# Kernel tuning notes

Measured on AMD Instinct MI355X. Metric: run time of the kernel, lower is better.

## Reference

```python
import jax, jax.numpy as jnp
import numpy as np

EPS = 1e-5


def _conv(x, w, pad, groups=1):
    return jax.lax.conv_general_dilated(
        x, w, (1, 1), [(pad, pad), (pad, pad)],
        dimension_numbers=('NCHW', 'OIHW', 'NCHW'),
        feature_group_count=groups)


def _bn(x, p):
    # p: [4, C] = (gamma, beta, running_mean, running_var); eval-mode BatchNorm2d
    g, b, m, v = p
    scale = g / jnp.sqrt(v + EPS)
    return x * scale[None, :, None, None] + (b - m * scale)[None, :, None, None]


def _deform_sample(ir, offset, mask):
    # ir: [B,C,H,W]; offset: [B,18,H,W] interleaved (dy,dx) per 3x3 tap; mask: [B,9,H,W]
    B, C, H, W = ir.shape
    K = 9
    off = offset.reshape(B, K, 2, H, W)
    ky, kx = jnp.meshgrid(jnp.arange(3) - 1, jnp.arange(3) - 1, indexing='ij')
    ys = off[:, :, 0] + ky.reshape(K).astype(ir.dtype)[None, :, None, None] \
         + jnp.arange(H, dtype=ir.dtype)[None, None, :, None]
    xs = off[:, :, 1] + kx.reshape(K).astype(ir.dtype)[None, :, None, None] \
         + jnp.arange(W, dtype=ir.dtype)[None, None, None, :]

    def sample_one(img, ys_b, xs_b):
        # img [C,H,W]; ys_b/xs_b [K,H,W] -> [C,K,H,W]
        y0 = jnp.floor(ys_b); x0 = jnp.floor(xs_b)
        wy = ys_b - y0; wx = xs_b - x0
        y0i = y0.astype(jnp.int32); x0i = x0.astype(jnp.int32)

        def gather(yi, xi):
            valid = (yi >= 0) & (yi < H) & (xi >= 0) & (xi < W)
            v = img[:, jnp.clip(yi, 0, H - 1), jnp.clip(xi, 0, W - 1)]
            return v * valid[None].astype(img.dtype)

        return (gather(y0i, x0i) * ((1 - wy) * (1 - wx))[None]
                + gather(y0i, x0i + 1) * ((1 - wy) * wx)[None]
                + gather(y0i + 1, x0i) * (wy * (1 - wx))[None]
                + gather(y0i + 1, x0i + 1) * (wy * wx)[None])

    vals = jax.vmap(sample_one)(ir, ys, xs)  # [B,C,K,H,W]
    return vals * mask[:, None]  # modulated (DCNv2) sampling


def reference(rgb, ir, w_off1, b_off1, w_off2, b_off2, w_dcn, b_dcn,
              w_g1, bn_g1, w_g2, bn_g2, w_g3, b_g3, w_f, bn_f, res_scale):
    silu = jax.nn.silu
    cat = jnp.concatenate([rgb, ir], axis=1)
    h = silu(_conv(cat, w_off1, 1) + b_off1[None, :, None, None])
    out = _conv(h, w_off2, 1) + b_off2[None, :, None, None]  # [B,27,H,W]
    o1, o2, m = jnp.split(out, 3, axis=1)
    offset = jnp.concatenate([o1, o2], axis=1)  # [B,18,H,W]
    mask = jax.nn.sigmoid(m)                    # [B,9,H,W]

    vals = _deform_sample(ir, offset, mask)     # [B,C,9,H,W]
    Co = w_dcn.shape[0]
    ir_aligned = jnp.einsum('bckhw,ock->bohw', vals, w_dcn.reshape(Co, -1, 9)) \
                 + b_dcn[None, :, None, None]

    mid = w_g2.shape[0]
    g = silu(_bn(_conv(jnp.concatenate([rgb, ir_aligned], axis=1), w_g1, 0), bn_g1))
    g = silu(_bn(_conv(g, w_g2, 1, groups=mid), bn_g2))
    g = jax.nn.sigmoid(_conv(g, w_g3, 0) + b_g3[None, :, None, None])  # [B,1,H,W]

    fused_in = jnp.concatenate([g * ir_aligned, (1.0 - g) * rgb], axis=1)
    fused = silu(_bn(_conv(fused_in, w_f, 1), bn_f))
    return fused + res_scale * ir_aligned


def setup_inputs() -> dict:
    B, CH, H, W = 8, 128, 80, 80
    MID = max(CH // 8, 16)
    key = jax.random.key(0)
    ks = jax.random.split(key, 20)

    def bn_params(k, c):
        k1, k2, k3, k4 = jax.random.split(k, 4)
        gamma = 1.0 + 0.1 * jax.random.normal(k1, (c,), jnp.float32)
        beta = 0.1 * jax.random.normal(k2, (c,), jnp.float32)
        mean = 0.1 * jax.random.normal(k3, (c,), jnp.float32)
        var = jax.random.uniform(k4, (c,), jnp.float32, 0.5, 1.5)
        return jnp.stack([gamma, beta, mean, var])

    return {
        'rgb': jax.random.normal(ks[0], (B, CH, H, W), jnp.float32),
        'ir': jax.random.normal(ks[1], (B, CH, H, W), jnp.float32),
        'w_off1': 0.02 * jax.random.normal(ks[2], (CH, 2 * CH, 3, 3), jnp.float32),
        'b_off1': 0.02 * jax.random.normal(ks[3], (CH,), jnp.float32),
        'w_off2': 0.01 * jax.random.normal(ks[4], (27, CH, 3, 3), jnp.float32),
        'b_off2': 0.01 * jax.random.normal(ks[5], (27,), jnp.float32),
        'w_dcn': 0.03 * jax.random.normal(ks[6], (CH, CH, 3, 3), jnp.float32),
        'b_dcn': 0.03 * jax.random.normal(ks[7], (CH,), jnp.float32),
        'w_g1': 0.05 * jax.random.normal(ks[8], (MID, 2 * CH, 1, 1), jnp.float32),
        'bn_g1': bn_params(ks[9], MID),
        'w_g2': 0.1 * jax.random.normal(ks[10], (MID, 1, 3, 3), jnp.float32),
        'bn_g2': bn_params(ks[11], MID),
        'w_g3': 0.1 * jax.random.normal(ks[12], (1, MID, 1, 1), jnp.float32),
        'b_g3': jnp.ones((1,), jnp.float32),
        'w_f': 0.03 * jax.random.normal(ks[13], (CH, 2 * CH, 3, 3), jnp.float32),
        'bn_f': bn_params(ks[14], CH),
        'res_scale': jnp.array(0.2, jnp.float32),
    }
```

## Files before the change

kernel.cpp:

```cpp
#include <hip/hip_runtime.h>
#include <math.h>

#define HWs 6400

typedef __attribute__((ext_vector_type(8))) short s8v;
typedef __attribute__((ext_vector_type(4))) float f4v;
typedef unsigned short ushortT;
typedef unsigned int uintT;

__device__ __forceinline__ float sigm_(float x){ return 1.0f/(1.0f+__expf(-x)); }
__device__ __forceinline__ float silu_(float x){ return x/(1.0f+__expf(-x)); }
__device__ __forceinline__ ushortT f2bf(float f){
  uintT u = __float_as_uint(f);
  u = (u + 0x7fffu + ((u>>16)&1u)) >> 16;
  return (ushortT)u;
}

__global__ void wtb_kernel(const float* __restrict__ w, ushortT* __restrict__ Bt,
                           int lcin, int OC, int Npad, int K){
  int idx = blockIdx.x*256 + threadIdx.x;
  if (idx >= Npad*K) return;
  int n = idx / K, k = idx - n*K;
  int r = k >> lcin, c = k & ((1<<lcin)-1);
  float v = (n < OC) ? w[(((size_t)n << lcin) + c)*9 + r] : 0.0f;
  Bt[idx] = f2bf(v);
}

__global__ void bnprep_kernel(const float* __restrict__ bn1, const float* __restrict__ bn2,
                              const float* __restrict__ bnf, float* __restrict__ o){
  int t = threadIdx.x;
  if (t < 16){
    float s = bn1[t] / sqrtf(bn1[48+t] + 1e-5f);
    o[t] = s; o[16+t] = bn1[16+t] - bn1[32+t]*s;
  } else if (t < 32){
    int i = t-16;
    float s = bn2[i] / sqrtf(bn2[48+i] + 1e-5f);
    o[32+i] = s; o[48+i] = bn2[16+i] - bn2[32+i]*s;
  } else if (t < 160){
    int i = t-32;
    float s = bnf[i] / sqrtf(bnf[384+i] + 1e-5f);
    o[64+i] = s; o[192+i] = bnf[128+i] - bnf[256+i]*s;
  }
}

template<int MODE, int BN, int EPI, int LCIN>
__global__ __launch_bounds__(256,4)
void mconv(const float* __restrict__ A0, const float* __restrict__ A1,
           int Cin0,
           const float* __restrict__ offp,
           const ushortT* __restrict__ Bt, int K,
           float* __restrict__ Out, int Nout,
           const float* __restrict__ e0, const float* __restrict__ e1,
           const float* __restrict__ res, const float* __restrict__ rsp)
{
  constexpr int CINM = (1<<LCIN) - 1;
  constexpr int MF = (BN==128)? 2 : 1;
  constexpr int NF = (BN==128)? 4 : 2;
  constexpr int BCH = (BN==128)? 2 : 1;
  __shared__ ushortT As[64*40];
  __shared__ ushortT Bs[BN*40];

  const int tid = threadIdx.x;
  const int mb  = blockIdx.x * 64;
  const int b   = mb / HWs;
  const int sm  = tid & 63;
  const int kg  = tid >> 6;
  const int p   = mb - b*HWs + sm;
  const int y   = p / 80;
  const int x   = p - y*80;

  const float* a0p = A0 + (size_t)b*Cin0*HWs + p;
  const float* a1p = (MODE!=1)? (A1 + ((size_t)b*((1<<LCIN)-Cin0) - (size_t)Cin0)*HWs + p) : A0;
  const float* gp  = (MODE==2)? (offp + (size_t)b*HWs + p) : A0;
  const float* ofb = (MODE==1)? (offp + (size_t)b*27*HWs + p) : A0;
  const float* irb = A0 + (size_t)b*128*HWs;

  const int ln  = tid & 63;
  const int l15 = ln & 15, lg = ln >> 4;
  const int wv  = tid >> 6;
  const int wmb = (BN==128)? ((wv>>1)*32) : (wv*16);
  const int wnb = (BN==128)? ((wv&1)*64) : 0;

  f4v acc[MF][NF];
  #pragma unroll
  for (int i=0;i<MF;i++)
    #pragma unroll
    for (int j=0;j<NF;j++)
      #pragma unroll
      for (int q=0;q<4;q++) acc[i][j][q] = 0.0f;

  float w00=0.f,w01=0.f,w10=0.f,w11=0.f;
  int o00=0,o01=0,o10=0,o11=0;
  float gvr = 0.f;

  for (int k0 = 0; k0 < K; k0 += 32){
    const int kb = k0 + kg*8;
    const int r  = kb >> LCIN;
    const int c0 = kb & CINM;
    s8v h;

    if (MODE != 1){
      const int r3 = r/3;
      const int dy = r3 - 1, dx = r - r3*3 - 1;
      const int yy = y + dy, xx = x + dx;
      const bool v = ((unsigned)yy < 80u) & ((unsigned)xx < 80u);
      const float* bp = (c0 < Cin0)? a0p : a1p;
      const float* q = bp + (size_t)c0*HWs + (dy*80 + dx);
      float scl = 1.0f;
      if (MODE == 2){
        if ((k0 & CINM) == 0){
          gvr = v ? gp[dy*80 + dx] : 0.0f;
        }
        scl = (c0 < Cin0)? gvr : (1.0f - gvr);
      }
      if (v){
        #pragma unroll
        for (int kk=0;kk<8;kk++){
          float val = q[(size_t)kk*HWs];
          if (MODE == 2) val *= scl;
          h[kk] = (short)f2bf(val);
        }
      } else {
        #pragma unroll
        for (int kk=0;kk<8;kk++) h[kk] = 0;
      }
    } else {
      if ((k0 & 127) == 0){
        float oy = ofb[(size_t)(2*r)*HWs];
        float ox = ofb[(size_t)(2*r+1)*HWs];
        float mk = sigm_(ofb[(size_t)(18+r)*HWs]);
        int r3 = r/3;
        int dy = r3, dx = r - r3*3;
        float ys = oy + (float)(y + dy - 1);
        float xs = ox + (float)(x + dx - 1);
        float yf = floorf(ys), xf = floorf(xs);
        float wy = ys - yf, wx = xs - xf;
        int y0 = (int)yf, x0 = (int)xf;
        float vy0 = ((unsigned)y0     < 80u)? 1.f : 0.f;
        float vy1 = ((unsigned)(y0+1) < 80u)? 1.f : 0.f;
        float vx0 = ((unsigned)x0     < 80u)? 1.f : 0.f;
        float vx1 = ((unsigned)(x0+1) < 80u)? 1.f : 0.f;
        w00 = (1.f-wy)*(1.f-wx)*mk*vy0*vx0;
        w01 = (1.f-wy)*wx      *mk*vy0*vx1;
        w10 = wy      *(1.f-wx)*mk*vy1*vx0;
        w11 = wy      *wx      *mk*vy1*vx1;
        int cy0 = min(max(y0  ,0),79), cy1 = min(max(y0+1,0),79);
        int cx0 = min(max(x0  ,0),79), cx1 = min(max(x0+1,0),79);
        o00 = cy0*80+cx0; o01 = cy0*80+cx1; o10 = cy1*80+cx0; o11 = cy1*80+cx1;
      }
      const float* q00 = irb + (size_t)c0*HWs + o00;
      const float* q01 = irb + (size_t)c0*HWs + o01;
      const float* q10 = irb + (size_t)c0*HWs + o10;
      const float* q11 = irb + (size_t)c0*HWs + o11;
      #pragma unroll
      for (int kk=0;kk<8;kk++){
        float val = w00*q00[(size_t)kk*HWs] + w01*q01[(size_t)kk*HWs]
                  + w10*q10[(size_t)kk*HWs] + w11*q11[(size_t)kk*HWs];
        h[kk] = (short)f2bf(val);
      }
    }

    uint4 bchunk[BCH];
    #pragma unroll
    for (int i=0;i<BCH;i++){
      int ch = tid + i*256;
      if (BN==128 || tid < 128){
        int n = ch >> 2, kc = (ch & 3) << 3;
        bchunk[i] = *(const uint4*)(Bt + (size_t)n*K + k0 + kc);
      }
    }

    __syncthreads();
    *(s8v*)&As[sm*40 + kg*8] = h;
    #pragma unroll
    for (int i=0;i<BCH;i++){
      int ch = tid + i*256;
      if (BN==128 || tid < 128){
        int n = ch >> 2, kc = (ch & 3) << 3;
        *(uint4*)&Bs[n*40 + kc] = bchunk[i];
      }
    }
    __syncthreads();

    s8v af[MF], bfr[NF];
    #pragma unroll
    for (int i=0;i<MF;i++) af[i]  = *(const s8v*)&As[(wmb + i*16 + l15)*40 + lg*8];
    #pragma unroll
    for (int j=0;j<NF;j++) bfr[j] = *(const s8v*)&Bs[(wnb + j*16 + l15)*40 + lg*8];
    #pragma unroll
    for (int i=0;i<MF;i++)
      #pragma unroll
      for (int j=0;j<NF;j++)
        acc[i][j] = __builtin_amdgcn_mfma_f32_16x16x32_bf16(af[i], bfr[j], acc[i][j], 0, 0, 0);
    __syncthreads();
  }

  float rsv = (EPI==3)? rsp[0] : 0.0f;
  #pragma unroll
  for (int i=0;i<MF;i++){
    int p0 = (mb - b*HWs) + wmb + i*16 + 4*lg;
    #pragma unroll
    for (int j=0;j<NF;j++){
      int n = wnb + j*16 + l15;
      if (BN==32 && n >= Nout) continue;
      size_t ob = ((size_t)b*Nout + n)*HWs + p0;
      float vv[4];
      #pragma unroll
      for (int q=0;q<4;q++) vv[q] = acc[i][j][q];
      if (EPI == 0){
        float bb = e0[n];
        #pragma unroll
        for (int q=0;q<4;q++) vv[q] += bb;
      } else if (EPI == 1){
        float bb = e0[n];
        #pragma unroll
        for (int q=0;q<4;q++) vv[q] = silu_(vv[q] + bb);
      } else if (EPI == 2){
        float s = e0[n], sh = e1[n];
        #pragma unroll
        for (int q=0;q<4;q++) vv[q] = silu_(fmaf(vv[q], s, sh));
      } else {
        float s = e0[n], sh = e1[n];
        float4 r4 = *(const float4*)(res + ob);
        float rr[4] = {r4.x, r4.y, r4.z, r4.w};
        #pragma unroll
        for (int q=0;q<4;q++) vv[q] = silu_(fmaf(vv[q], s, sh)) + rsv*rr[q];
      }
      float4 o4; o4.x=vv[0]; o4.y=vv[1]; o4.z=vv[2]; o4.w=vv[3];
      *(float4*)(Out + ob) = o4;
    }
  }
}

__global__ __launch_bounds__(256) void gate1_kernel(
  const float* __restrict__ rgb, const float* __restrict__ iral,
  const float* __restrict__ wg1, const float* __restrict__ bns,
  float* __restrict__ out)
{
  __shared__ float Ws[4096];
  int tid = threadIdx.x;
  for (int i = tid; i < 4096; i += 256){
    int mc = i >> 8, c = i & 255;
    Ws[c*16 + mc] = wg1[i];
  }
  __syncthreads();
  int idx = blockIdx.x*256 + tid;
  int b = idx / HWs, p = idx - b*HWs;
  const float* r0 = rgb  + (size_t)b*128*HWs + p;
  const float* i0 = iral + ((size_t)b*128 - 128)*HWs + p;
  float acc[16];
  #pragma unroll
  for (int mc=0;mc<16;mc++) acc[mc]=0.f;
  #pragma unroll 4
  for (int c=0;c<256;c++){
    float v = (c<128) ? r0[(size_t)c*HWs] : i0[(size_t)c*HWs];
    const float4* w4 = (const float4*)&Ws[c*16];
    #pragma unroll
    for (int q=0;q<4;q++){
      float4 w = w4[q];
      acc[q*4+0] = fmaf(v, w.x, acc[q*4+0]);
      acc[q*4+1] = fmaf(v, w.y, acc[q*4+1]);
      acc[q*4+2] = fmaf(v, w.z, acc[q*4+2]);
      acc[q*4+3] = fmaf(v, w.w, acc[q*4+3]);
    }
  }
  #pragma unroll
  for (int mc=0;mc<16;mc++){
    float t = fmaf(acc[mc], bns[mc], bns[16+mc]);
    out[((size_t)b*16+mc)*HWs + p] = silu_(t);
  }
}

__global__ __launch_bounds__(256) void gate23_kernel(
  const float* __restrict__ g1b, const float* __restrict__ wg2,
  const float* __restrict__ wg3, const float* __restrict__ bg3,
  const float* __restrict__ bns, float* __restrict__ g)
{
  __shared__ float w2s[144], w3s[16], sc2[16], sh2[16];
  __shared__ float b3s;
  int tid = threadIdx.x;
  if (tid < 144) w2s[tid] = wg2[tid];
  if (tid < 16){ w3s[tid] = wg3[tid]; sc2[tid] = bns[32+tid]; sh2[tid] = bns[48+tid]; }
  if (tid == 0) b3s = bg3[0];
  __syncthreads();
  int idx = blockIdx.x*256 + tid;
  int b = idx / HWs, p = idx - b*HWs;
  int y = p/80, x = p - y*80;
  float acc = b3s;
  #pragma unroll
  for (int mc=0;mc<16;mc++){
    const float* base = g1b + ((size_t)b*16+mc)*HWs;
    float s = 0.f;
    #pragma unroll
    for (int r=0;r<9;r++){
      int dy = r/3, dx = r - (r/3)*3;
      int yy = y + dy - 1, xx = x + dx - 1;
      if (((unsigned)yy < 80u) & ((unsigned)xx < 80u))
        s = fmaf(base[yy*80+xx], w2s[mc*9+r], s);
    }
    float t = fmaf(s, sc2[mc], sh2[mc]);
    acc = fmaf(silu_(t), w3s[mc], acc);
  }
  g[idx] = sigm_(acc);
}

extern "C" void kernel_launch(void* const* d_in, const int* in_sizes, int n_in,
                              void* d_out, int out_size, void* d_ws, size_t ws_size,
                              hipStream_t stream)
{
  const float* rgb  = (const float*)d_in[0];
  const float* ir   = (const float*)d_in[1];
  const float* w1   = (const float*)d_in[2];
  const float* b1   = (const float*)d_in[3];
  const float* w2   = (const float*)d_in[4];
  const float* b2   = (const float*)d_in[5];
  const float* wd   = (const float*)d_in[6];
  const float* bd   = (const float*)d_in[7];
  const float* wg1  = (const float*)d_in[8];
  const float* bng1 = (const float*)d_in[9];
  const float* wg2  = (const float*)d_in[10];
  const float* bng2 = (const float*)d_in[11];
  const float* wg3  = (const float*)d_in[12];
  const float* bg3  = (const float*)d_in[13];
  const float* wf   = (const float*)d_in[14];
  const float* bnf  = (const float*)d_in[15];
  const float* rs   = (const float*)d_in[16];
  float* out = (float*)d_out;

  float* ws   = (float*)d_ws;
  float* hbuf = ws;
  float* offb = hbuf + 6553600;
  float* iral = offb + 1382400;
  float* g1b  = iral + 6553600;
  float* gbuf = g1b  + 819200;
  float* bns  = gbuf + 51200;
  ushortT* Bt1 = (ushortT*)(bns + 320);
  ushortT* Bt2 = Bt1 + 294912;
  ushortT* Bt3 = Bt2 + 36864;
  ushortT* Bt4 = Bt3 + 147456;

  bnprep_kernel<<<1, 256, 0, stream>>>(bng1, bng2, bnf, bns);
  wtb_kernel<<<(294912+255)/256, 256, 0, stream>>>(w1, Bt1, 8, 128, 128, 2304);
  wtb_kernel<<<( 36864+255)/256, 256, 0, stream>>>(w2, Bt2, 7,  27,  32, 1152);
  wtb_kernel<<<(147456+255)/256, 256, 0, stream>>>(wd, Bt3, 7, 128, 128, 1152);
  wtb_kernel<<<(294912+255)/256, 256, 0, stream>>>(wf, Bt4, 8, 128, 128, 2304);

  mconv<0,128,1,8><<<800, 256, 0, stream>>>(rgb, ir, 128, nullptr,
      Bt1, 2304, hbuf, 128, b1, nullptr, nullptr, nullptr);
  mconv<0,32,0,7><<<800, 256, 0, stream>>>(hbuf, hbuf, 128, nullptr,
      Bt2, 1152, offb, 27, b2, nullptr, nullptr, nullptr);
  mconv<1,128,0,7><<<800, 256, 0, stream>>>(ir, ir, 128, offb,
      Bt3, 1152, iral, 128, bd, nullptr, nullptr, nullptr);
  gate1_kernel<<<200, 256, 0, stream>>>(rgb, iral, wg1, bns, g1b);
  gate23_kernel<<<200, 256, 0, stream>>>(g1b, wg2, wg3, bg3, bns, gbuf);
  mconv<2,128,3,8><<<800, 256, 0, stream>>>(iral, rgb, 128, gbuf,
      Bt4, 2304, out, 128, bns+64, bns+192, iral, rs);
}
```

Measured before the change: 928.9 us.

## Reorder im2col K as channel-major with taps padded to sixteen

Changes the GEMM K ordering for the regular 3x3 convolutions so that each channel's 9 taps sit in a 16-wide slot. Each thread loads 8 taps from one channel plane instead of 8 channels at one tap, which gives spatially local loads and per-tap bounds checks. The price is K growing from 2304 to 4096 (and 1152 to 2048), so roughly 78% more MFMA work is spent on zero padding. Blocks are also reindexed so that adjacent block IDs cover different batch images at the same spatial tile. The gate value is now loaded per tap rather than once per tap group.

```diff
diff --git a/kernel.cpp b/kernel.cpp
--- a/kernel.cpp
+++ b/kernel.cpp
@@ -17,12 +17,20 @@
 }
 
 __global__ void wtb_kernel(const float* __restrict__ w, ushortT* __restrict__ Bt,
-                           int lcin, int OC, int Npad, int K){
+                           int lcin, int OC, int Npad, int K, int pad16){
   int idx = blockIdx.x*256 + threadIdx.x;
   if (idx >= Npad*K) return;
   int n = idx / K, k = idx - n*K;
-  int r = k >> lcin, c = k & ((1<<lcin)-1);
-  float v = (n < OC) ? w[(((size_t)n << lcin) + c)*9 + r] : 0.0f;
+  float v = 0.0f;
+  if (n < OC){
+    if (pad16){
+      int c = k >> 4, r = k & 15;
+      if (r < 9) v = w[(((size_t)n << lcin) + c)*9 + r];
+    } else {
+      int r = k >> lcin, c = k & ((1<<lcin)-1);
+      v = w[(((size_t)n << lcin) + c)*9 + r];
+    }
+  }
   Bt[idx] = f2bf(v);
 }
 
@@ -61,19 +69,22 @@
   __shared__ ushortT Bs[BN*40];
 
   const int tid = threadIdx.x;
-  const int mb  = blockIdx.x * 64;
-  const int b   = mb / HWs;
+  const int bid = blockIdx.x;
+  const int b   = bid & 7;
+  const int pt  = (bid >> 3) * 64;
   const int sm  = tid & 63;
   const int kg  = tid >> 6;
-  const int p   = mb - b*HWs + sm;
+  const int cg  = kg >> 1;
+  const int hi  = kg & 1;
+  const int p   = pt + sm;
   const int y   = p / 80;
   const int x   = p - y*80;
 
-  const float* a0p = A0 + (size_t)b*Cin0*HWs + p;
-  const float* a1p = (MODE!=1)? (A1 + ((size_t)b*((1<<LCIN)-Cin0) - (size_t)Cin0)*HWs + p) : A0;
-  const float* gp  = (MODE==2)? (offp + (size_t)b*HWs + p) : A0;
-  const float* ofb = (MODE==1)? (offp + (size_t)b*27*HWs + p) : A0;
-  const float* irb = A0 + (size_t)b*128*HWs;
+  const float* base0 = A0 + (size_t)b*Cin0*HWs;
+  const float* base1 = (MODE!=1)? (A1 + ((size_t)b*((1<<LCIN)-Cin0) - (size_t)Cin0)*HWs) : A0;
+  const float* gb    = (MODE==2)? (offp + (size_t)b*HWs) : A0;
+  const float* ofb   = (MODE==1)? (offp + (size_t)b*27*HWs + p) : A0;
+  const float* irb   = A0 + (size_t)b*128*HWs;
 
   const int ln  = tid & 63;
   const int l15 = ln & 15, lg = ln >> 4;
@@ -91,40 +102,42 @@
 
   float w00=0.f,w01=0.f,w10=0.f,w11=0.f;
   int o00=0,o01=0,o10=0,o11=0;
-  float gvr = 0.f;
 
   for (int k0 = 0; k0 < K; k0 += 32){
-    const int kb = k0 + kg*8;
-    const int r  = kb >> LCIN;
-    const int c0 = kb & CINM;
     s8v h;
-
     if (MODE != 1){
-      const int r3 = r/3;
-      const int dy = r3 - 1, dx = r - r3*3 - 1;
-      const int yy = y + dy, xx = x + dx;
-      const bool v = ((unsigned)yy < 80u) & ((unsigned)xx < 80u);
-      const float* bp = (c0 < Cin0)? a0p : a1p;
-      const float* q = bp + (size_t)c0*HWs + (dy*80 + dx);
-      float scl = 1.0f;
-      if (MODE == 2){
-        if ((k0 & CINM) == 0){
-          gvr = v ? gp[dy*80 + dx] : 0.0f;
-        }
-        scl = (c0 < Cin0)? gvr : (1.0f - gvr);
-      }
-      if (v){
-        #pragma unroll
-        for (int kk=0;kk<8;kk++){
-          float val = q[(size_t)kk*HWs];
-          if (MODE == 2) val *= scl;
-          h[kk] = (short)f2bf(val);
+      const int c = (k0 >> 4) + cg;
+      const float* plane = ((c < Cin0)? base0 : base1) + (size_t)c*HWs;
+      if (hi == 0){
+        #pragma unroll
+        for (int kk=0; kk<8; kk++){
+          const int dyc = kk/3 - 1;
+          const int dxc = kk - (kk/3)*3 - 1;
+          const bool v = ((unsigned)(y+dyc) < 80u) & ((unsigned)(x+dxc) < 80u);
+          const int pp = v ? (p + dyc*80 + dxc) : 0;
+          float val = plane[pp];
+          if (MODE == 2){
+            float gv = gb[pp];
+            val *= (c < Cin0)? gv : (1.0f - gv);
+          }
+          h[kk] = (short)(v ? f2bf(val) : (ushortT)0);
         }
       } else {
-        #pragma unroll
-        for (int kk=0;kk<8;kk++) h[kk] = 0;
+        const bool v = ((unsigned)(y+1) < 80u) & ((unsigned)(x+1) < 80u);
+        const int pp = v ? (p + 81) : 0;
+        float val = plane[pp];
+        if (MODE == 2){
+          float gv = gb[pp];
+          val *= (c < Cin0)? gv : (1.0f - gv);
+        }
+        h[0] = (short)(v ? f2bf(val) : (ushortT)0);
+        #pragma unroll
+        for (int kk=1; kk<8; kk++) h[kk] = 0;
       }
     } else {
+      const int kb = k0 + kg*8;
+      const int r  = kb >> 7;
+      const int c0 = kb & 127;
       if ((k0 & 127) == 0){
         float oy = ofb[(size_t)(2*r)*HWs];
         float ox = ofb[(size_t)(2*r+1)*HWs];
@@ -198,7 +211,7 @@
   float rsv = (EPI==3)? rsp[0] : 0.0f;
   #pragma unroll
   for (int i=0;i<MF;i++){
-    int p0 = (mb - b*HWs) + wmb + i*16 + 4*lg;
+    int p0 = pt + wmb + i*16 + 4*lg;
     #pragma unroll
     for (int j=0;j<NF;j++){
       int n = wnb + j*16 + l15;
@@ -335,24 +348,24 @@
   float* gbuf = g1b  + 819200;
   float* bns  = gbuf + 51200;
   ushortT* Bt1 = (ushortT*)(bns + 320);
-  ushortT* Bt2 = Bt1 + 294912;
-  ushortT* Bt3 = Bt2 + 36864;
+  ushortT* Bt2 = Bt1 + 524288;
+  ushortT* Bt3 = Bt2 + 65536;
   ushortT* Bt4 = Bt3 + 147456;
 
   bnprep_kernel<<<1, 256, 0, stream>>>(bng1, bng2, bnf, bns);
-  wtb_kernel<<<(294912+255)/256, 256, 0, stream>>>(w1, Bt1, 8, 128, 128, 2304);
-  wtb_kernel<<<( 36864+255)/256, 256, 0, stream>>>(w2, Bt2, 7,  27,  32, 1152);
-  wtb_kernel<<<(147456+255)/256, 256, 0, stream>>>(wd, Bt3, 7, 128, 128, 1152);
-  wtb_kernel<<<(294912+255)/256, 256, 0, stream>>>(wf, Bt4, 8, 128, 128, 2304);
+  wtb_kernel<<<(524288+255)/256, 256, 0, stream>>>(w1, Bt1, 8, 128, 128, 4096, 1);
+  wtb_kernel<<<( 65536+255)/256, 256, 0, stream>>>(w2, Bt2, 7,  27,  32, 2048, 1);
+  wtb_kernel<<<(147456+255)/256, 256, 0, stream>>>(wd, Bt3, 7, 128, 128, 1152, 0);
+  wtb_kernel<<<(524288+255)/256, 256, 0, stream>>>(wf, Bt4, 8, 128, 128, 4096, 1);
 
   mconv<0,128,1,8><<<800, 256, 0, stream>>>(rgb, ir, 128, nullptr,
-      Bt1, 2304, hbuf, 128, b1, nullptr, nullptr, nullptr);
+      Bt1, 4096, hbuf, 128, b1, nullptr, nullptr, nullptr);
   mconv<0,32,0,7><<<800, 256, 0, stream>>>(hbuf, hbuf, 128, nullptr,
-      Bt2, 1152, offb, 27, b2, nullptr, nullptr, nullptr);
+      Bt2, 2048, offb, 27, b2, nullptr, nullptr, nullptr);
   mconv<1,128,0,7><<<800, 256, 0, stream>>>(ir, ir, 128, offb,
       Bt3, 1152, iral, 128, bd, nullptr, nullptr, nullptr);
   gate1_kernel<<<200, 256, 0, stream>>>(rgb, iral, wg1, bns, g1b);
   gate23_kernel<<<200, 256, 0, stream>>>(g1b, wg2, wg3, bg3, bns, gbuf);
   mconv<2,128,3,8><<<800, 256, 0, stream>>>(iral, rgb, 128, gbuf,
-      Bt4, 2304, out, 128, bns+64, bns+192, iral, rs);
-}
+      Bt4, 4096, out, 128, bns+64, bns+192, iral, rs);
+}
```

New measurement: 1.337 ms. +44.0%, slower.
